# Performance work log

Measured on AMD Instinct MI355X. Metric: run time of the kernel, lower is better.

Reference implementation:

```python
import jax, jax.numpy as jnp
import numpy as np

B, N, C = 2, 3072, 768
H = 12                      # num_heads
HD = C // H                 # 64
D = HD // 2                 # 32, rope dim per axis
GRID_H, GRID_W = 48, 64     # 768/16, 1024/16 ; GRID_H*GRID_W == N
BASE = 100.0
EPS = 1e-5


def _rope_tables():
    # positions per token (row-major cartesian product of y,x)
    pos_y = np.repeat(np.arange(GRID_H), GRID_W)   # [N]
    pos_x = np.tile(np.arange(GRID_W), GRID_H)     # [N]
    seq_len = max(GRID_H, GRID_W)
    inv_freq = 1.0 / BASE ** (np.arange(0, D, 2, dtype=np.float32) / D)  # [D/2]
    t = np.arange(seq_len, dtype=np.float32)
    freqs = np.einsum('i,j->ij', t, inv_freq)            # [S, D/2]
    emb = np.concatenate([freqs, freqs], axis=-1)        # [S, D]
    cos, sin = np.cos(emb), np.sin(emb)
    # gather per-token, add head broadcast dims -> [1, 1, N, D]
    mk = lambda tbl, idx: jnp.asarray(tbl[idx][None, None], dtype=jnp.float32)
    return mk(cos, pos_x), mk(sin, pos_x), mk(cos, pos_y), mk(sin, pos_y)


def setup_inputs() -> dict:
    key = jax.random.key(0)
    ks = jax.random.split(key, 12)
    s = 0.02
    cos_x, sin_x, cos_y, sin_y = _rope_tables()
    return {
        'x': jax.random.normal(ks[0], (B, N, C), jnp.float32),
        'w_qkv': jax.random.normal(ks[1], (3 * C, C), jnp.float32) * s,
        'w_proj': jax.random.normal(ks[2], (C, C), jnp.float32) * s,
        'b_proj': jnp.zeros((C,), jnp.float32),
        'g1': jnp.ones((C,), jnp.float32),
        'beta1': jnp.zeros((C,), jnp.float32),
        'g2': jnp.ones((C,), jnp.float32),
        'beta2': jnp.zeros((C,), jnp.float32),
        'w_fc1': jax.random.normal(ks[3], (4 * C, C), jnp.float32) * s,
        'b_fc1': jnp.zeros((4 * C,), jnp.float32),
        'w_fc2': jax.random.normal(ks[4], (C, 4 * C), jnp.float32) * s,
        'b_fc2': jnp.zeros((C,), jnp.float32),
        'cos_x': cos_x, 'sin_x': sin_x, 'cos_y': cos_y, 'sin_y': sin_y,
    }


def _layernorm(x, g, b):
    m = x.mean(-1, keepdims=True)
    v = ((x - m) ** 2).mean(-1, keepdims=True)
    return (x - m) * jax.lax.rsqrt(v + EPS) * g + b


def _rope1d(tok, cos, sin):
    t1, t2 = jnp.split(tok, 2, axis=-1)
    rot = jnp.concatenate([-t2, t1], axis=-1)
    return tok * cos + rot * sin


def _rope2d(tok, cos_x, sin_x, cos_y, sin_y):
    # tok: [B, H, N, HD]; first half of HD is y-coords, second half x-coords
    ty, tx = jnp.split(tok, 2, axis=-1)
    return jnp.concatenate([_rope1d(ty, cos_y, sin_y), _rope1d(tx, cos_x, sin_x)], axis=-1)


def reference(x, w_qkv, w_proj, b_proj, g1, beta1, g2, beta2,
              w_fc1, b_fc1, w_fc2, b_fc2, cos_x, sin_x, cos_y, sin_y):
    # --- attention branch ---
    xn = _layernorm(x, g1, beta1)
    qkv = jnp.einsum('bnc,dc->bnd', xn, w_qkv)           # [B, N, 3C]
    qkv = qkv.reshape(B, N, 3, H, HD).transpose(0, 3, 2, 1, 4)  # [B, H, 3, N, HD]
    q, k, v = qkv[:, :, 0], qkv[:, :, 1], qkv[:, :, 2]
    q = _rope2d(q, cos_x, sin_x, cos_y, sin_y)
    k = _rope2d(k, cos_x, sin_x, cos_y, sin_y)
    scale = HD ** -0.5
    attn = jnp.einsum('bhqd,bhkd->bhqk', q, k) * scale   # [B, H, N, N]
    attn = jax.nn.softmax(attn, axis=-1)
    o = jnp.einsum('bhqk,bhkd->bhqd', attn, v)           # [B, H, N, HD]
    o = o.transpose(0, 2, 1, 3).reshape(B, N, C)
    o = jnp.einsum('bnc,dc->bnd', o, w_proj) + b_proj
    x = x + o
    # --- mlp branch ---
    xn = _layernorm(x, g2, beta2)
    h = jnp.einsum('bnc,hc->bnh', xn, w_fc1) + b_fc1
    h = jax.nn.gelu(h, approximate=False)                # torch nn.GELU default (erf)
    h = jnp.einsum('bnh,ch->bnc', h, w_fc2) + b_fc2
    return x + h
```

## Files before the change

### kernel.cpp

```cpp
#include <hip/hip_runtime.h>
#include <hip/hip_bf16.h>


#define Nn 3072
#define Cc 768
#define Hh 12
#define Mm 6144

typedef unsigned short ushort_t;
typedef unsigned int u32;
using s8v = __attribute__((ext_vector_type(8))) short;
using f4v = __attribute__((ext_vector_type(4))) float;

__device__ __forceinline__ ushort_t f2b(float x){
  u32 u = __float_as_uint(x);
  return (ushort_t)((u + 0x7fffu + ((u >> 16) & 1u)) >> 16);
}
__device__ __forceinline__ u32 pack2(float a, float b){
  return (u32)f2b(a) | ((u32)f2b(b) << 16);
}
__device__ __forceinline__ u32 pack2t(float a, float b){
  return (__float_as_uint(a) >> 16) | (__float_as_uint(b) & 0xffff0000u);
}
__device__ __forceinline__ float b2f(ushort_t u){
  return __uint_as_float(((u32)u) << 16);
}

#define GLD16(g, l) __builtin_amdgcn_global_load_lds( \
    (const __attribute__((address_space(1))) u32*)(g), \
    (__attribute__((address_space(3))) u32*)(l), 16, 0, 0)

__global__ __launch_bounds__(256) void cvt4_kernel(
    const float* __restrict__ a, ushort_t* __restrict__ oa, int na,
    const float* __restrict__ b, ushort_t* __restrict__ ob, int nb,
    const float* __restrict__ c, ushort_t* __restrict__ oc, int nc,
    const float* __restrict__ d, ushort_t* __restrict__ od)
{
  int i = (blockIdx.x*256 + threadIdx.x)*4;
  const float* src; ushort_t* dst;
  if (i < na)           { src = a + i;            dst = oa + i; }
  else if (i < na+nb)   { src = b + (i-na);       dst = ob + (i-na); }
  else if (i < na+nb+nc){ src = c + (i-na-nb);    dst = oc + (i-na-nb); }
  else                  { src = d + (i-na-nb-nc); dst = od + (i-na-nb-nc); }
  float4 v = *(const float4*)src;
  uint2 p; p.x = pack2(v.x, v.y); p.y = pack2(v.z, v.w);
  *(uint2*)dst = p;
}

__global__ __launch_bounds__(256) void ln_kernel(const float* __restrict__ in,
    const float* __restrict__ g, const float* __restrict__ be, ushort_t* __restrict__ out)
{
  int row = blockIdx.x;
  int tid = threadIdx.x;
  size_t base = (size_t)row * Cc;
  float v[3];
  #pragma unroll
  for (int i = 0; i < 3; ++i) v[i] = in[base + tid + i*256];
  __shared__ float red[8];
  float s = v[0]+v[1]+v[2];
  #pragma unroll
  for (int off=32; off; off>>=1) s += __shfl_xor(s, off);
  int wid = tid >> 6, lane = tid & 63;
  if (lane==0) red[wid] = s;
  __syncthreads();
  float mean = (red[0]+red[1]+red[2]+red[3]) * (1.f/Cc);
  float d = 0.f;
  #pragma unroll
  for (int i=0;i<3;++i){ float t = v[i]-mean; d += t*t; }
  #pragma unroll
  for (int off=32; off; off>>=1) d += __shfl_xor(d, off);
  if (lane==0) red[4+wid] = d;
  __syncthreads();
  float var  = (red[4]+red[5]+red[6]+red[7]) * (1.f/Cc);
  float rstd = rsqrtf(var + 1e-5f);
  #pragma unroll
  for (int i=0;i<3;++i){
    int idx = tid + i*256;
    out[base+idx] = f2b((v[i]-mean)*rstd*g[idx] + be[idx]);
  }
}

template<int EPI, int NT>
__global__ __launch_bounds__(256) void mgemm_kernel(
    const ushort_t* __restrict__ A, const ushort_t* __restrict__ W,
    const float* __restrict__ bias, const float* __restrict__ residf,
    void* __restrict__ outv, int Nd, int K)
{
  constexpr int JT = NT/32;
  __shared__ __align__(16) ushort_t As[128*32];
  __shared__ __align__(16) ushort_t Ws[NT*32];
  int tid = threadIdx.x;
  int w = tid >> 6, lane = tid & 63;
  int g = lane >> 4, c = lane & 15;
  int wr = w >> 1, wc = w & 1;
  int m0 = blockIdx.y * 128, n0 = blockIdx.x * NT;
  int schunk = (lane & 3) * 8;
  const ushort_t* Ag = A + (size_t)(m0 + w*32 + (lane >> 2))*K + schunk;
  const ushort_t* Wg;
  if constexpr (NT == 128) Wg = W + (size_t)(n0 + w*32 + (lane >> 2))*K + schunk;
  else                     Wg = W + (size_t)(n0 + w*16 + (lane >> 2))*K + schunk;
  ushort_t* Asl = &As[w*1024];
  ushort_t* Wsl = (NT == 128) ? &Ws[w*1024] : &Ws[w*512];
  f4v acc[4][JT] = {};
  for (int k0 = 0; k0 < K; k0 += 32) {
    __syncthreads();
    GLD16(Ag + k0,        Asl);
    GLD16(Ag + 16*K + k0, Asl + 512);
    GLD16(Wg + k0,        Wsl);
    if constexpr (NT == 128) GLD16(Wg + 16*K + k0, Wsl + 512);
    __syncthreads();
    s8v af[4], wf[JT];
    #pragma unroll
    for (int i=0;i<4;++i) af[i] = *(const s8v*)&As[(wr*64 + i*16 + c)*32 + g*8];
    #pragma unroll
    for (int j=0;j<JT;++j) wf[j] = *(const s8v*)&Ws[(wc*(NT/2) + j*16 + c)*32 + g*8];
    #pragma unroll
    for (int i=0;i<4;++i)
      #pragma unroll
      for (int j=0;j<JT;++j)
        acc[i][j] = __builtin_amdgcn_mfma_f32_16x16x32_bf16(af[i], wf[j], acc[i][j], 0,0,0);
  }
  #pragma unroll
  for (int j=0;j<JT;++j){
    int col = n0 + wc*(NT/2) + j*16 + c;
    float bv = (EPI != 0) ? bias[col] : 0.f;
    #pragma unroll
    for (int i=0;i<4;++i){
      int row0 = m0 + wr*64 + i*16 + g*4;
      #pragma unroll
      for (int r=0;r<4;++r){
        float v = acc[i][j][r];
        size_t off = (size_t)(row0 + r)*Nd + col;
        if (EPI == 0) {
          ((ushort_t*)outv)[off] = f2b(v);
        } else if (EPI == 2) {
          float t = v + bv;
          ((ushort_t*)outv)[off] = f2b(0.5f*t*(1.0f + erff(t*0.70710678118654752f)));
        } else {
          ((float*)outv)[off] = v + bv + residf[off];
        }
      }
    }
  }
}

__global__ __launch_bounds__(256) void repack_kernel(
    const ushort_t* __restrict__ qkv,
    const float* __restrict__ cx, const float* __restrict__ sx,
    const float* __restrict__ cy, const float* __restrict__ sy,
    ushort_t* __restrict__ Qb, ushort_t* __restrict__ Kb, ushort_t* __restrict__ Vt)
{
  __shared__ float Vls[64*68];
  int bh = blockIdx.y;
  int b = bh / Hh, h = bh - b*Hh;
  int n0 = blockIdx.x * 64;
  int tid = threadIdx.x;
  int tt = tid >> 2, cch = tid & 3;
  int n = n0 + tt;
  size_t rowbase = (size_t)(b*Nn + n) * 2304 + h*64;

  int half = cch >> 1, ibase = (cch & 1) * 8;
  int d1 = half*32 + ibase;
  const float* ct  = half ? cx : cy;
  const float* st_ = half ? sx : sy;
  float c1[8], s1[8], c2[8], s2[8];
  #pragma unroll
  for (int j=0;j<8;++j){
    c1[j] = ct[n*32 + ibase + j];       s1[j] = st_[n*32 + ibase + j];
    c2[j] = ct[n*32 + ibase + 16 + j];  s2[j] = st_[n*32 + ibase + 16 + j];
  }
  #pragma unroll
  for (int qk = 0; qk < 2; ++qk){
    const ushort_t* src = qkv + rowbase + qk*768;
    uint4 uv1 = *(const uint4*)(src + d1);
    uint4 uv2 = *(const uint4*)(src + d1 + 16);
    float v1[8], v2[8];
    v1[0]=b2f(uv1.x&0xffff); v1[1]=b2f(uv1.x>>16); v1[2]=b2f(uv1.y&0xffff); v1[3]=b2f(uv1.y>>16);
    v1[4]=b2f(uv1.z&0xffff); v1[5]=b2f(uv1.z>>16); v1[6]=b2f(uv1.w&0xffff); v1[7]=b2f(uv1.w>>16);
    v2[0]=b2f(uv2.x&0xffff); v2[1]=b2f(uv2.x>>16); v2[2]=b2f(uv2.y&0xffff); v2[3]=b2f(uv2.y>>16);
    v2[4]=b2f(uv2.z&0xffff); v2[5]=b2f(uv2.z>>16); v2[6]=b2f(uv2.w&0xffff); v2[7]=b2f(uv2.w>>16);
    float sc = qk ? 1.0f : 0.18033688011112042f;
    float o1[8], o2[8];
    #pragma unroll
    for (int j=0;j<8;++j){
      o1[j] = (v1[j]*c1[j] - v2[j]*s1[j]) * sc;
      o2[j] = (v2[j]*c2[j] + v1[j]*s2[j]) * sc;
    }
    ushort_t* dst = (qk ? Kb : Qb) + ((size_t)bh*Nn + n)*64;
    uint4 u1, u2;
    u1.x = pack2(o1[0],o1[1]); u1.y = pack2(o1[2],o1[3]);
    u1.z = pack2(o1[4],o1[5]); u1.w = pack2(o1[6],o1[7]);
    u2.x = pack2(o2[0],o2[1]); u2.y = pack2(o2[2],o2[3]);
    u2.z = pack2(o2[4],o2[5]); u2.w = pack2(o2[6],o2[7]);
    *(uint4*)(dst + d1)      = u1;
    *(uint4*)(dst + d1 + 16) = u2;
  }

  {
    const ushort_t* src = qkv + rowbase + 1536 + cch*16;
    uint4 ua = *(const uint4*)(src);
    uint4 ub = *(const uint4*)(src + 8);
    float* lp = &Vls[tt*68 + cch*16];
    lp[0]=b2f(ua.x&0xffff); lp[1]=b2f(ua.x>>16); lp[2]=b2f(ua.y&0xffff); lp[3]=b2f(ua.y>>16);
    lp[4]=b2f(ua.z&0xffff); lp[5]=b2f(ua.z>>16); lp[6]=b2f(ua.w&0xffff); lp[7]=b2f(ua.w>>16);
    lp[8]=b2f(ub.x&0xffff); lp[9]=b2f(ub.x>>16); lp[10]=b2f(ub.y&0xffff); lp[11]=b2f(ub.y>>16);
    lp[12]=b2f(ub.z&0xffff); lp[13]=b2f(ub.z>>16); lp[14]=b2f(ub.w&0xffff); lp[15]=b2f(ub.w>>16);
  }
  __syncthreads();
  {
    int d = tid & 63, quarter = tid >> 6;
    float v[16];
    #pragma unroll
    for (int j=0;j<16;++j) v[j] = Vls[(quarter*16 + j)*68 + d];
    uint4 w0, w1;
    w0.x = pack2(v[0],v[1]);   w0.y = pack2(v[2],v[3]);
    w0.z = pack2(v[4],v[5]);   w0.w = pack2(v[6],v[7]);
    w1.x = pack2(v[8],v[9]);   w1.y = pack2(v[10],v[11]);
    w1.z = pack2(v[12],v[13]); w1.w = pack2(v[14],v[15]);
    ushort_t* dst = Vt + ((size_t)bh*64 + d)*Nn + n0 + quarter*16;
    *(uint4*)(dst)     = w0;
    *(uint4*)(dst + 8) = w1;
  }
}

__global__ __launch_bounds__(256, 3) void fattn_kernel(
    const ushort_t* __restrict__ Qb, const ushort_t* __restrict__ Kb,
    const ushort_t* __restrict__ Vt, ushort_t* __restrict__ ob)
{
  __shared__ __align__(16) char smem[36864];
  __shared__ float Lred[256];
  int bh = blockIdx.x;
  int q0 = blockIdx.y * 64;
  int tid = threadIdx.x;
  int w = tid >> 6, lane = tid & 63, g = lane >> 4, c = lane & 15;

  const ushort_t* kbase = Kb + (size_t)bh*Nn*64;
  const ushort_t* vbase = Vt + (size_t)bh*64*Nn;

  s8v qf0[4], qf1[4];
  #pragma unroll
  for (int qs=0;qs<4;++qs){
    const ushort_t* qp = Qb + ((size_t)bh*Nn + q0 + qs*16 + c)*64;
    qf0[qs] = *(const s8v*)(qp + g*8);
    qf1[qs] = *(const s8v*)(qp + 32 + g*8);
  }
  s8v ones8;
  #pragma unroll
  for (int j=0;j<8;++j) ones8[j] = (short)0x3f80;

  f4v o[4][4] = {};
  f4v l[4] = {};
  ushort_t* pw = (ushort_t*)smem + w*4608;

  for (int it = 0; it < 12; ++it){
    int key0 = (it*4 + w) * 64;
    s8v ka[4], kb2[4];
    #pragma unroll
    for (int ks=0;ks<4;++ks){
      const ushort_t* kr = kbase + (size_t)(key0 + ks*16 + c)*64 + g*8;
      ka[ks]  = *(const s8v*)(kr);
      kb2[ks] = *(const s8v*)(kr + 32);
    }
    #pragma unroll
    for (int qs=0;qs<4;++qs){
      #pragma unroll
      for (int ks=0;ks<4;++ks){
        f4v z = {0,0,0,0};
        z = __builtin_amdgcn_mfma_f32_16x16x32_bf16(ka[ks],  qf0[qs], z, 0,0,0);
        z = __builtin_amdgcn_mfma_f32_16x16x32_bf16(kb2[ks], qf1[qs], z, 0,0,0);
        uint2 pk;
        pk.x = pack2t(__builtin_amdgcn_exp2f(z[0]), __builtin_amdgcn_exp2f(z[1]));
        pk.y = pack2t(__builtin_amdgcn_exp2f(z[2]), __builtin_amdgcn_exp2f(z[3]));
        *(uint2*)&pw[qs*1152 + c*72 + ks*16 + g*4] = pk;
      }
    }
    asm volatile("s_waitcnt lgkmcnt(0)" ::: "memory");
    s8v va[4], vb[4];
    #pragma unroll
    for (int d=0;d<4;++d){
      const ushort_t* vr = vbase + (size_t)(d*16 + c)*Nn + key0 + g*8;
      va[d] = *(const s8v*)(vr);
      vb[d] = *(const s8v*)(vr + 32);
    }
    #pragma unroll
    for (int qs=0;qs<4;++qs){
      s8v pf0 = *(const s8v*)&pw[qs*1152 + c*72 + g*8];
      s8v pf1 = *(const s8v*)&pw[qs*1152 + c*72 + 32 + g*8];
      #pragma unroll
      for (int d=0;d<4;++d){
        o[qs][d] = __builtin_amdgcn_mfma_f32_16x16x32_bf16(va[d], pf0, o[qs][d], 0,0,0);
        o[qs][d] = __builtin_amdgcn_mfma_f32_16x16x32_bf16(vb[d], pf1, o[qs][d], 0,0,0);
      }
      l[qs] = __builtin_amdgcn_mfma_f32_16x16x32_bf16(ones8, pf0, l[qs], 0,0,0);
      l[qs] = __builtin_amdgcn_mfma_f32_16x16x32_bf16(ones8, pf1, l[qs], 0,0,0);
    }
  }

  ushort_t* Or = (ushort_t*)smem;
  #pragma unroll
  for (int qs=0;qs<4;++qs){
    #pragma unroll
    for (int d=0;d<4;++d){
      uint2 pk;
      pk.x = pack2(o[qs][d][0], o[qs][d][1]);
      pk.y = pack2(o[qs][d][2], o[qs][d][3]);
      *(uint2*)&Or[(w*64 + qs*16 + c)*72 + d*16 + g*4] = pk;
    }
    Lred[w*64 + qs*16 + c] = l[qs][0];
  }
  __syncthreads();

  int qrow = tid >> 2, dseg = (tid & 3) * 16;
  float acc[16] = {};
  #pragma unroll
  for (int w2=0;w2<4;++w2){
    const ushort_t* base = &Or[(w2*64 + qrow)*72 + dseg];
    uint4 u0 = *(const uint4*)(base);
    uint4 u1 = *(const uint4*)(base + 8);
    u32 uu[8] = {u0.x,u0.y,u0.z,u0.w,u1.x,u1.y,u1.z,u1.w};
    #pragma unroll
    for (int j=0;j<8;++j){
      acc[j*2]   += b2f((ushort_t)(uu[j] & 0xffff));
      acc[j*2+1] += b2f((ushort_t)(uu[j] >> 16));
    }
  }
  float rl = 1.0f / (Lred[qrow] + Lred[64+qrow] + Lred[128+qrow] + Lred[192+qrow]);
  int b = bh / Hh, h = bh - b*Hh;
  ushort_t* op = ob + ((size_t)b*Nn + q0 + qrow)*768 + h*64 + dseg;
  uint4 w0_, w1_;
  w0_.x = pack2(acc[0]*rl, acc[1]*rl);   w0_.y = pack2(acc[2]*rl, acc[3]*rl);
  w0_.z = pack2(acc[4]*rl, acc[5]*rl);   w0_.w = pack2(acc[6]*rl, acc[7]*rl);
  w1_.x = pack2(acc[8]*rl, acc[9]*rl);   w1_.y = pack2(acc[10]*rl, acc[11]*rl);
  w1_.z = pack2(acc[12]*rl, acc[13]*rl); w1_.w = pack2(acc[14]*rl, acc[15]*rl);
  *(uint4*)(op)     = w0_;
  *(uint4*)(op + 8) = w1_;
}

extern "C" void kernel_launch(void* const* d_in, const int* in_sizes, int n_in,
                              void* d_out, int out_size, void* d_ws, size_t ws_size,
                              hipStream_t stream)
{
  const float* x      = (const float*)d_in[0];
  const float* w_qkv  = (const float*)d_in[1];
  const float* w_proj = (const float*)d_in[2];
  const float* b_proj = (const float*)d_in[3];
  const float* g1     = (const float*)d_in[4];
  const float* be1    = (const float*)d_in[5];
  const float* g2     = (const float*)d_in[6];
  const float* be2    = (const float*)d_in[7];
  const float* w_fc1  = (const float*)d_in[8];
  const float* b_fc1  = (const float*)d_in[9];
  const float* w_fc2  = (const float*)d_in[10];
  const float* b_fc2  = (const float*)d_in[11];
  const float* cx     = (const float*)d_in[12];
  const float* sx     = (const float*)d_in[13];
  const float* cy     = (const float*)d_in[14];
  const float* sy     = (const float*)d_in[15];
  float* out = (float*)d_out;

  char* ws = (char*)d_ws;
  ushort_t* xnb   = (ushort_t*)(ws);
  ushort_t* Qb    = (ushort_t*)(ws + 9437184);
  ushort_t* Kb    = (ushort_t*)(ws + 18874368);
  float*    x1    = (float*)   (ws + 9437184);
  ushort_t* Vt    = (ushort_t*)(ws + 28311552);
  ushort_t* obb   = (ushort_t*)(ws + 37748736);
  ushort_t* qkvb  = (ushort_t*)(ws + 47185920);
  ushort_t* hb    = (ushort_t*)(ws + 47185920);
  ushort_t* wqkvb = (ushort_t*)(ws + 84934656);
  ushort_t* wprojb= (ushort_t*)(ws + 88473600);
  ushort_t* wfc1b = (ushort_t*)(ws + 89653248);
  ushort_t* wfc2b = (ushort_t*)(ws + 94371840);

  cvt4_kernel<<<(7077888/4)/256, 256, 0, stream>>>(
      w_qkv, wqkvb, 2304*768, w_proj, wprojb, 768*768,
      w_fc1, wfc1b, 3072*768, w_fc2, wfc2b);

  ln_kernel<<<Mm, 256, 0, stream>>>(x, g1, be1, xnb);
  mgemm_kernel<0,128><<<dim3(2304/128, Mm/128), 256, 0, stream>>>(xnb, wqkvb, nullptr, nullptr, qkvb, 2304, 768);
  repack_kernel<<<dim3(48, 24), 256, 0, stream>>>(qkvb, cx, sx, cy, sy, Qb, Kb, Vt);
  fattn_kernel<<<dim3(24, 48), 256, 0, stream>>>(Qb, Kb, Vt, obb);
  mgemm_kernel<1,64><<<dim3(768/64, Mm/128), 256, 0, stream>>>(obb, wprojb, b_proj, x, x1, 768, 768);
  ln_kernel<<<Mm, 256, 0, stream>>>(x1, g2, be2, xnb);
  mgemm_kernel<2,128><<<dim3(3072/128, Mm/128), 256, 0, stream>>>(xnb, wfc1b, b_fc1, nullptr, hb, 3072, 768);
  mgemm_kernel<1,64><<<dim3(768/64, Mm/128), 256, 0, stream>>>(hb, wfc2b, b_fc2, x1, out, 768, 3072);
}
```

Before: 455.6 us.

## Split attention waves across query halves and key halves, compute row sums with VALU

The flash-attention kernel's four waves now form a 2x2 grid: each handles 32 query rows over half of the keys in 32-key steps, where before each took all 64 queries over a quarter of the keys. Softmax row sums come from VALU adds plus cross-lane shuffles instead of extra MFMAs against a ones vector. Shared memory shrinks, launch bounds rise to 4 blocks per CU, and the final reduction merges only two partials. The intent is higher occupancy, less LDS and register pressure, and fewer redundant MFMAs, at the cost of more loop iterations with less work each.

Measured after the change: 554.4 us. 21.7% more time.

```diff
diff --git a/kernel.cpp b/kernel.cpp
--- a/kernel.cpp
+++ b/kernel.cpp
@@ -223,98 +223,100 @@
   }
 }
 
-__global__ __launch_bounds__(256, 3) void fattn_kernel(
+__global__ __launch_bounds__(256, 4) void fattn_kernel(
     const ushort_t* __restrict__ Qb, const ushort_t* __restrict__ Kb,
     const ushort_t* __restrict__ Vt, ushort_t* __restrict__ ob)
 {
-  __shared__ __align__(16) char smem[36864];
-  __shared__ float Lred[256];
+  __shared__ __align__(16) ushort_t OrS[2*64*72];
+  __shared__ float Lred[128];
   int bh = blockIdx.x;
   int q0 = blockIdx.y * 64;
   int tid = threadIdx.x;
   int w = tid >> 6, lane = tid & 63, g = lane >> 4, c = lane & 15;
+  int wq = w >> 1, wk = w & 1;
 
   const ushort_t* kbase = Kb + (size_t)bh*Nn*64;
   const ushort_t* vbase = Vt + (size_t)bh*64*Nn;
 
-  s8v qf0[4], qf1[4];
-  #pragma unroll
-  for (int qs=0;qs<4;++qs){
-    const ushort_t* qp = Qb + ((size_t)bh*Nn + q0 + qs*16 + c)*64;
+  s8v qf0[2], qf1[2];
+  #pragma unroll
+  for (int qs=0;qs<2;++qs){
+    const ushort_t* qp = Qb + ((size_t)bh*Nn + q0 + wq*32 + qs*16 + c)*64;
     qf0[qs] = *(const s8v*)(qp + g*8);
     qf1[qs] = *(const s8v*)(qp + 32 + g*8);
   }
-  s8v ones8;
-  #pragma unroll
-  for (int j=0;j<8;++j) ones8[j] = (short)0x3f80;
-
-  f4v o[4][4] = {};
-  f4v l[4] = {};
-  ushort_t* pw = (ushort_t*)smem + w*4608;
-
-  for (int it = 0; it < 12; ++it){
-    int key0 = (it*4 + w) * 64;
-    s8v ka[4], kb2[4];
-    #pragma unroll
-    for (int ks=0;ks<4;++ks){
+
+  f4v o[2][4] = {};
+  float s0 = 0.f, s1 = 0.f;
+  ushort_t* pw = OrS + w*1280;
+
+  int kb0 = wk*1536;
+  for (int it = 0; it < 48; ++it){
+    int key0 = kb0 + it*32;
+    s8v va[4];
+    #pragma unroll
+    for (int d=0;d<4;++d)
+      va[d] = *(const s8v*)(vbase + (size_t)(d*16 + c)*Nn + key0 + g*8);
+    s8v ka[2], kb2[2];
+    #pragma unroll
+    for (int ks=0;ks<2;++ks){
       const ushort_t* kr = kbase + (size_t)(key0 + ks*16 + c)*64 + g*8;
       ka[ks]  = *(const s8v*)(kr);
       kb2[ks] = *(const s8v*)(kr + 32);
     }
     #pragma unroll
-    for (int qs=0;qs<4;++qs){
+    for (int qs=0;qs<2;++qs){
       #pragma unroll
-      for (int ks=0;ks<4;++ks){
+      for (int ks=0;ks<2;++ks){
         f4v z = {0,0,0,0};
         z = __builtin_amdgcn_mfma_f32_16x16x32_bf16(ka[ks],  qf0[qs], z, 0,0,0);
         z = __builtin_amdgcn_mfma_f32_16x16x32_bf16(kb2[ks], qf1[qs], z, 0,0,0);
-        uint2 pk;
-        pk.x = pack2t(__builtin_amdgcn_exp2f(z[0]), __builtin_amdgcn_exp2f(z[1]));
-        pk.y = pack2t(__builtin_amdgcn_exp2f(z[2]), __builtin_amdgcn_exp2f(z[3]));
-        *(uint2*)&pw[qs*1152 + c*72 + ks*16 + g*4] = pk;
+        float e0 = __builtin_amdgcn_exp2f(z[0]);
+        float e1 = __builtin_amdgcn_exp2f(z[1]);
+        float e2 = __builtin_amdgcn_exp2f(z[2]);
+        float e3 = __builtin_amdgcn_exp2f(z[3]);
+        float es = (e0+e1)+(e2+e3);
+        if (qs) s1 += es; else s0 += es;
+        uint2 pk; pk.x = pack2t(e0,e1); pk.y = pack2t(e2,e3);
+        *(uint2*)&pw[qs*640 + c*40 + ks*16 + g*4] = pk;
       }
     }
-    asm volatile("s_waitcnt lgkmcnt(0)" ::: "memory");
-    s8v va[4], vb[4];
-    #pragma unroll
-    for (int d=0;d<4;++d){
-      const ushort_t* vr = vbase + (size_t)(d*16 + c)*Nn + key0 + g*8;
-      va[d] = *(const s8v*)(vr);
-      vb[d] = *(const s8v*)(vr + 32);
-    }
-    #pragma unroll
-    for (int qs=0;qs<4;++qs){
-      s8v pf0 = *(const s8v*)&pw[qs*1152 + c*72 + g*8];
-      s8v pf1 = *(const s8v*)&pw[qs*1152 + c*72 + 32 + g*8];
+    #pragma unroll
+    for (int qs=0;qs<2;++qs){
+      s8v pf = *(const s8v*)&pw[qs*640 + c*40 + g*8];
       #pragma unroll
-      for (int d=0;d<4;++d){
-        o[qs][d] = __builtin_amdgcn_mfma_f32_16x16x32_bf16(va[d], pf0, o[qs][d], 0,0,0);
-        o[qs][d] = __builtin_amdgcn_mfma_f32_16x16x32_bf16(vb[d], pf1, o[qs][d], 0,0,0);
-      }
-      l[qs] = __builtin_amdgcn_mfma_f32_16x16x32_bf16(ones8, pf0, l[qs], 0,0,0);
-      l[qs] = __builtin_amdgcn_mfma_f32_16x16x32_bf16(ones8, pf1, l[qs], 0,0,0);
-    }
-  }
-
-  ushort_t* Or = (ushort_t*)smem;
-  #pragma unroll
-  for (int qs=0;qs<4;++qs){
+      for (int d=0;d<4;++d)
+        o[qs][d] = __builtin_amdgcn_mfma_f32_16x16x32_bf16(va[d], pf, o[qs][d], 0,0,0);
+    }
+  }
+
+  s0 += __shfl_xor(s0, 16); s0 += __shfl_xor(s0, 32);
+  s1 += __shfl_xor(s1, 16); s1 += __shfl_xor(s1, 32);
+
+  __syncthreads();
+
+  #pragma unroll
+  for (int qs=0;qs<2;++qs){
+    int row = wk*64 + wq*32 + qs*16 + c;
     #pragma unroll
     for (int d=0;d<4;++d){
       uint2 pk;
       pk.x = pack2(o[qs][d][0], o[qs][d][1]);
       pk.y = pack2(o[qs][d][2], o[qs][d][3]);
-      *(uint2*)&Or[(w*64 + qs*16 + c)*72 + d*16 + g*4] = pk;
-    }
-    Lred[w*64 + qs*16 + c] = l[qs][0];
+      *(uint2*)&OrS[row*72 + d*16 + g*4] = pk;
+    }
+  }
+  if (g == 0){
+    Lred[wk*64 + wq*32 + c]      = s0;
+    Lred[wk*64 + wq*32 + 16 + c] = s1;
   }
   __syncthreads();
 
   int qrow = tid >> 2, dseg = (tid & 3) * 16;
   float acc[16] = {};
   #pragma unroll
-  for (int w2=0;w2<4;++w2){
-    const ushort_t* base = &Or[(w2*64 + qrow)*72 + dseg];
+  for (int w2=0;w2<2;++w2){
+    const ushort_t* base = &OrS[(w2*64 + qrow)*72 + dseg];
     uint4 u0 = *(const uint4*)(base);
     uint4 u1 = *(const uint4*)(base + 8);
     u32 uu[8] = {u0.x,u0.y,u0.z,u0.w,u1.x,u1.y,u1.z,u1.w};
@@ -324,7 +326,7 @@
       acc[j*2+1] += b2f((ushort_t)(uu[j] >> 16));
     }
   }
-  float rl = 1.0f / (Lred[qrow] + Lred[64+qrow] + Lred[128+qrow] + Lred[192+qrow]);
+  float rl = 1.0f / (Lred[qrow] + Lred[64+qrow]);
   int b = bh / Hh, h = bh - b*Hh;
   ushort_t* op = ob + ((size_t)b*Nn + q0 + qrow)*768 + h*64 + dseg;
   uint4 w0_, w1_;
```
